# Kernel tuning notes

Measured on AMD Instinct MI355X. Metric: run time of the kernel, lower is better.

## Reference

```python
import jax, jax.numpy as jnp
import numpy as np

B, I, A, H = 64, 128, 16, 1024
E = int(0.8 * H)           # excitatory columns (819)
DT = 0.02
ALPHA_X = DT / 0.1         # dt/tau_x = 0.2
ALPHA_W = DT / 1.0         # dt/tau_w = 0.02
WBOUND = 1.0


def _make_mask_h():
    # EI sign mask: +1 for excitatory cols, -1 for inhibitory; zero diagonal (remove_diag=True)
    sign = jnp.concatenate([jnp.ones(E), -jnp.ones(H - E)])
    return jnp.broadcast_to(sign[None, :], (H, H)) * (1.0 - jnp.eye(H))


def setup_inputs() -> dict:
    key = jax.random.key(0)
    ks = jax.random.split(key, 11)
    return dict(
        x=jax.random.normal(ks[0], (B, I), dtype=jnp.float32),
        state=jax.random.normal(ks[1], (B, H), dtype=jnp.float32),
        output=jax.random.uniform(ks[2], (B, H), dtype=jnp.float32),
        wh=jax.random.uniform(ks[3], (B, H, H), dtype=jnp.float32) * 0.05,
        da=jax.random.normal(ks[4], (B,), dtype=jnp.float32),
        aux_x=jax.random.normal(ks[5], (B, A), dtype=jnp.float32),
        W_x=jax.random.normal(ks[6], (H, I), dtype=jnp.float32) * 0.05,
        W_aux=jax.random.normal(ks[7], (H, A), dtype=jnp.float32) * 0.05,
        W_h=jax.random.normal(ks[8], (H, H), dtype=jnp.float32) * 0.02,
        b_h=jax.random.normal(ks[9], (H,), dtype=jnp.float32) * 0.01,
        kappa=jax.random.uniform(ks[10], (H, H), dtype=jnp.float32) * 0.01,
        mask_h=_make_mask_h(),
    )


def reference(x, state, output, wh, da, aux_x, W_x, W_aux, W_h, b_h, kappa, mask_h):
    # input nonlinearities (sigma_in = 0, so no noise)
    x = jax.nn.relu(x)
    aux = jax.nn.relu(aux_x)
    # recurrent drive with per-sample plastic weight: effective_weight(w) = w * mask
    eff_wh = wh * mask_h[None]                                  # [B,H,H]
    total = jnp.einsum('bij,bj->bi', eff_wh, output) + b_h      # h2h (bias=True)
    # feedforward: pos_func = abs, mask = ones (e_prop=1, no zero cols)
    total = total + x @ jnp.abs(W_x).T + aux @ jnp.abs(W_aux).T
    # leaky integration (sigma_rec = 0)
    new_state = state * (1.0 - ALPHA_X) + total * ALPHA_X
    new_output = jnp.tanh(jax.nn.relu(new_state))               # retanh
    # additive Hebbian plasticity (plas_rule='add', sigma_w = 0)
    baseline = jnp.abs(W_h)[None]                               # [1,H,H]
    hebb = jnp.einsum('bi,bj->bij', new_output, new_output)     # post x pre
    new_w = (baseline * ALPHA_W + wh * (1.0 - ALPHA_W)
             + DT * da[:, None, None] * jnp.abs(kappa)[None] * hebb)
    new_w = jnp.clip(new_w, 0.0, WBOUND)
    return new_state, new_output, new_w
```

## Files before the change

kernel.cpp:

```cpp
#include <hip/hip_runtime.h>
#include <math.h>

#define BB 64
#define HH 1024
#define II 128
#define AA 16
#define ECOLS 819
#define ALPHA_X 0.2f
#define ALPHA_W 0.02f
#define DTC 0.02f

__global__ __launch_bounds__(1024) void phase1(
    const float* __restrict__ x, const float* __restrict__ state,
    const float* __restrict__ output, const float* __restrict__ wh,
    const float* __restrict__ da, const float* __restrict__ aux_x,
    const float* __restrict__ Wx, const float* __restrict__ Waux,
    const float* __restrict__ bh,
    float* __restrict__ new_state, float* __restrict__ new_output,
    float* __restrict__ crow)
{
    __shared__ float so[HH];
    __shared__ float xr[II];
    __shared__ float auxr[AA];

    const int tid   = threadIdx.x;
    const int b     = blockIdx.x >> 6;
    const int itile = blockIdx.x & 63;

    {
        float o = output[b * HH + tid];
        so[tid] = (tid < ECOLS) ? o : -o;
    }
    if (tid < II)  xr[tid]   = fmaxf(x[b * II + tid], 0.0f);
    if (tid < AA)  auxr[tid] = fmaxf(aux_x[b * AA + tid], 0.0f);
    __syncthreads();

    const int lane = tid & 63;
    const int w    = tid >> 6;
    const int i    = itile * 16 + w;

    const float* whrow = wh + ((size_t)b * HH + i) * HH;

    float acc = 0.0f;
    #pragma unroll
    for (int c = 0; c < 4; ++c) {
        int j = c * 256 + lane * 4;
        float4 a = reinterpret_cast<const float4*>(whrow + j)[0];
        float4 s = reinterpret_cast<const float4*>(so + j)[0];
        acc += a.x * s.x + a.y * s.y + a.z * s.z + a.w * s.w;
    }
    const float* wxr = Wx + (size_t)i * II;
    acc += xr[lane]      * fabsf(wxr[lane]);
    acc += xr[lane + 64] * fabsf(wxr[lane + 64]);
    if (lane < AA) acc += auxr[lane] * fabsf(Waux[(size_t)i * AA + lane]);

    #pragma unroll
    for (int off = 32; off > 0; off >>= 1)
        acc += __shfl_xor(acc, off);

    if (lane == 0) {
        float total = acc - whrow[i] * so[i] + bh[i];
        float ns = state[b * HH + i] * (1.0f - ALPHA_X) + total * ALPHA_X;
        float no = tanhf(fmaxf(ns, 0.0f));
        new_state[b * HH + i]  = ns;
        new_output[b * HH + i] = no;
        crow[b * HH + i]       = DTC * da[b] * no;
    }
}

__global__ __launch_bounds__(256) void phase2(
    const float* __restrict__ wh, const float* __restrict__ Whh,
    const float* __restrict__ kappa, const float* __restrict__ no,
    const float* __restrict__ crow, float* __restrict__ nw)
{
    const int N4 = BB * HH * (HH / 4);
    const int stride = gridDim.x * blockDim.x;
    int idx = blockIdx.x * blockDim.x + threadIdx.x;

    for (; idx < N4; idx += stride) {
        const int j4  = idx & 255;
        const int row = idx >> 8;
        const int i   = row & (HH - 1);
        const int b   = row >> 10;

        float4 wv = reinterpret_cast<const float4*>(wh)[idx];
        float4 wa = reinterpret_cast<const float4*>(Whh)[(i << 8) + j4];
        float4 ka = reinterpret_cast<const float4*>(kappa)[(i << 8) + j4];
        float4 nj = reinterpret_cast<const float4*>(no)[(b << 8) + j4];
        const float c = crow[row];

        float4 r;
        r.x = fminf(fmaxf(ALPHA_W * fabsf(wa.x) + (1.0f - ALPHA_W) * wv.x + c * fabsf(ka.x) * nj.x, 0.0f), 1.0f);
        r.y = fminf(fmaxf(ALPHA_W * fabsf(wa.y) + (1.0f - ALPHA_W) * wv.y + c * fabsf(ka.y) * nj.y, 0.0f), 1.0f);
        r.z = fminf(fmaxf(ALPHA_W * fabsf(wa.z) + (1.0f - ALPHA_W) * wv.z + c * fabsf(ka.z) * nj.z, 0.0f), 1.0f);
        r.w = fminf(fmaxf(ALPHA_W * fabsf(wa.w) + (1.0f - ALPHA_W) * wv.w + c * fabsf(ka.w) * nj.w, 0.0f), 1.0f);

        reinterpret_cast<float4*>(nw)[idx] = r;
    }
}

extern "C" void kernel_launch(void* const* d_in, const int* in_sizes, int n_in,
                              void* d_out, int out_size, void* d_ws, size_t ws_size,
                              hipStream_t stream) {
    const float* x      = (const float*)d_in[0];
    const float* state  = (const float*)d_in[1];
    const float* output = (const float*)d_in[2];
    const float* wh     = (const float*)d_in[3];
    const float* da     = (const float*)d_in[4];
    const float* aux_x  = (const float*)d_in[5];
    const float* Wx     = (const float*)d_in[6];
    const float* Waux   = (const float*)d_in[7];
    const float* Whh    = (const float*)d_in[8];
    const float* bh     = (const float*)d_in[9];
    const float* kappa  = (const float*)d_in[10];

    float* out        = (float*)d_out;
    float* new_state  = out;
    float* new_output = out + (size_t)BB * HH;
    float* new_w      = out + (size_t)2 * BB * HH;
    float* crow       = (float*)d_ws;

    phase1<<<dim3(BB * (HH / 16)), dim3(1024), 0, stream>>>(
        x, state, output, wh, da, aux_x, Wx, Waux, bh,
        new_state, new_output, crow);

    phase2<<<dim3(8192), dim3(256), 0, stream>>>(
        wh, Whh, kappa, new_output, crow, new_w);
}
```

Before: 545.5 us.

## Chunk batch into L2-sized pieces so phase2 rereads wh from cache

Processes the batch in chunks of 16, launching phase1 then phase2 per chunk, so the wh slice phase1 just streamed (64 MB per chunk) can still sit in the large last-level cache when phase2 reads it again. wh reads in phase2 and new_w writes are made nontemporal to limit cache pollution. This adds kernel launches and serialises the phases, and it relies on the chunk fitting in the MI355X Infinity Cache.

```diff
diff --git a/kernel.cpp b/kernel.cpp
--- a/kernel.cpp
+++ b/kernel.cpp
@@ -9,6 +9,9 @@
 #define ALPHA_X 0.2f
 #define ALPHA_W 0.02f
 #define DTC 0.02f
+#define CHUNK 16
+
+typedef float v4f __attribute__((ext_vector_type(4)));
 
 __global__ __launch_bounds__(1024) void phase1(
     const float* __restrict__ x, const float* __restrict__ state,
@@ -17,14 +20,14 @@
     const float* __restrict__ Wx, const float* __restrict__ Waux,
     const float* __restrict__ bh,
     float* __restrict__ new_state, float* __restrict__ new_output,
-    float* __restrict__ crow)
+    float* __restrict__ crow, int b0)
 {
     __shared__ float so[HH];
     __shared__ float xr[II];
     __shared__ float auxr[AA];
 
     const int tid   = threadIdx.x;
-    const int b     = blockIdx.x >> 6;
+    const int b     = b0 + (blockIdx.x >> 6);
     const int itile = blockIdx.x & 63;
 
     {
@@ -45,8 +48,8 @@
     #pragma unroll
     for (int c = 0; c < 4; ++c) {
         int j = c * 256 + lane * 4;
-        float4 a = reinterpret_cast<const float4*>(whrow + j)[0];
-        float4 s = reinterpret_cast<const float4*>(so + j)[0];
+        v4f a = *reinterpret_cast<const v4f*>(whrow + j);
+        v4f s = *reinterpret_cast<const v4f*>(so + j);
         acc += a.x * s.x + a.y * s.y + a.z * s.z + a.w * s.w;
     }
     const float* wxr = Wx + (size_t)i * II;
@@ -71,31 +74,33 @@
 __global__ __launch_bounds__(256) void phase2(
     const float* __restrict__ wh, const float* __restrict__ Whh,
     const float* __restrict__ kappa, const float* __restrict__ no,
-    const float* __restrict__ crow, float* __restrict__ nw)
+    const float* __restrict__ crow, float* __restrict__ nw, int b0)
 {
-    const int N4 = BB * HH * (HH / 4);
+    const int    N4    = CHUNK * HH * (HH / 4);
+    const size_t base4 = (size_t)b0 * HH * (HH / 4);
     const int stride = gridDim.x * blockDim.x;
     int idx = blockIdx.x * blockDim.x + threadIdx.x;
 
     for (; idx < N4; idx += stride) {
-        const int j4  = idx & 255;
-        const int row = idx >> 8;
-        const int i   = row & (HH - 1);
-        const int b   = row >> 10;
+        const int j4   = idx & 255;
+        const int lrow = idx >> 8;
+        const int i    = lrow & (HH - 1);
+        const int b    = b0 + (lrow >> 10);
+        const size_t g4 = base4 + idx;
 
-        float4 wv = reinterpret_cast<const float4*>(wh)[idx];
-        float4 wa = reinterpret_cast<const float4*>(Whh)[(i << 8) + j4];
-        float4 ka = reinterpret_cast<const float4*>(kappa)[(i << 8) + j4];
-        float4 nj = reinterpret_cast<const float4*>(no)[(b << 8) + j4];
-        const float c = crow[row];
+        v4f wv = __builtin_nontemporal_load(reinterpret_cast<const v4f*>(wh) + g4);
+        v4f wa = reinterpret_cast<const v4f*>(Whh)  [(i << 8) + j4];
+        v4f ka = reinterpret_cast<const v4f*>(kappa)[(i << 8) + j4];
+        v4f nj = reinterpret_cast<const v4f*>(no)   [((size_t)b << 8) + j4];
+        const float c = crow[(size_t)b * HH + i];
 
-        float4 r;
+        v4f r;
         r.x = fminf(fmaxf(ALPHA_W * fabsf(wa.x) + (1.0f - ALPHA_W) * wv.x + c * fabsf(ka.x) * nj.x, 0.0f), 1.0f);
         r.y = fminf(fmaxf(ALPHA_W * fabsf(wa.y) + (1.0f - ALPHA_W) * wv.y + c * fabsf(ka.y) * nj.y, 0.0f), 1.0f);
         r.z = fminf(fmaxf(ALPHA_W * fabsf(wa.z) + (1.0f - ALPHA_W) * wv.z + c * fabsf(ka.z) * nj.z, 0.0f), 1.0f);
         r.w = fminf(fmaxf(ALPHA_W * fabsf(wa.w) + (1.0f - ALPHA_W) * wv.w + c * fabsf(ka.w) * nj.w, 0.0f), 1.0f);
 
-        reinterpret_cast<float4*>(nw)[idx] = r;
+        __builtin_nontemporal_store(r, reinterpret_cast<v4f*>(nw) + g4);
     }
 }
 
@@ -120,10 +125,12 @@
     float* new_w      = out + (size_t)2 * BB * HH;
     float* crow       = (float*)d_ws;
 
-    phase1<<<dim3(BB * (HH / 16)), dim3(1024), 0, stream>>>(
-        x, state, output, wh, da, aux_x, Wx, Waux, bh,
-        new_state, new_output, crow);
+    for (int b0 = 0; b0 < BB; b0 += CHUNK) {
+        phase1<<<dim3(CHUNK * (HH / 16)), dim3(1024), 0, stream>>>(
+            x, state, output, wh, da, aux_x, Wx, Waux, bh,
+            new_state, new_output, crow, b0);
 
-    phase2<<<dim3(8192), dim3(256), 0, stream>>>(
-        wh, Whh, kappa, new_output, crow, new_w);
+        phase2<<<dim3(2048), dim3(256), 0, stream>>>(
+            wh, Whh, kappa, new_output, crow, new_w, b0);
+    }
 }
```

Result: faster. 512.6 us (-6.0%).
